# Kernel optimization log

Hardware: AMD Instinct MI355X
Metric: run time of the kernel (lower is better)

## Reference

```python
import jax, jax.numpy as jnp
import numpy as np

B, L, H, Q = 64, 512, 1024, 64
VA_H = 256


def setup_inputs() -> dict:
    key = jax.random.key(0)
    ks = jax.random.split(key, 10)
    hidden_states = jax.random.normal(ks[0], (B, L, H), dtype=jnp.float32)
    quad_spans = jax.random.randint(ks[1], (B, Q, 4), 0, L, dtype=jnp.int64)
    quad_mask = jnp.ones((B, Q), dtype=jnp.int32)
    s = 0.02
    W1 = jax.random.normal(ks[2], (3 * H, VA_H), dtype=jnp.float32) * s
    b1 = jnp.zeros((VA_H,), dtype=jnp.float32)
    W2 = jax.random.normal(ks[3], (VA_H, VA_H // 2), dtype=jnp.float32) * s
    b2 = jnp.zeros((VA_H // 2,), dtype=jnp.float32)
    W3 = jax.random.normal(ks[4], (VA_H // 2, 2), dtype=jnp.float32) * s
    b3 = jnp.zeros((2,), dtype=jnp.float32)
    return {"hidden_states": hidden_states, "quad_spans": quad_spans,
            "quad_mask": quad_mask, "W1": W1, "b1": b1, "W2": W2, "b2": b2,
            "W3": W3, "b3": b3}


def _pool_spans(hidden_states, quad_spans, quad_mask):
    # hidden_states [B,L,H]; quad_spans [B,Q,4]; quad_mask [B,Q]
    Bn, Ln, Hn = hidden_states.shape
    pos = jnp.arange(Ln)[None, None, :]                      # [1,1,L]
    asp_s = quad_spans[:, :, 0:1]
    asp_e = quad_spans[:, :, 1:2]
    opi_s = quad_spans[:, :, 2:3]
    opi_e = quad_spans[:, :, 3:4]
    asp_valid = asp_s >= 2
    opi_valid = opi_s >= 2
    sep = pos == 1                                           # [SEP] fallback
    asp_m = ((pos >= asp_s) & (pos <= asp_e) & asp_valid) | (~asp_valid & sep)
    opi_m = ((pos >= opi_s) & (pos <= opi_e) & opi_valid) | (~opi_valid & sep)
    qm = (quad_mask != 0)[:, :, None]
    asp_f = (asp_m & qm).astype(hidden_states.dtype)         # [B,Q,L]
    opi_f = (opi_m & qm).astype(hidden_states.dtype)
    h_asp = jnp.einsum('bql,blh->bqh', asp_f, hidden_states) / jnp.clip(
        asp_f.sum(-1, keepdims=True), 1.0, None)
    h_opi = jnp.einsum('bql,blh->bqh', opi_f, hidden_states) / jnp.clip(
        opi_f.sum(-1, keepdims=True), 1.0, None)
    return h_asp, h_opi


def reference(hidden_states, quad_spans, quad_mask, W1, b1, W2, b2, W3, b3):
    h_asp, h_opi = _pool_spans(hidden_states, quad_spans, quad_mask)
    h_pair = jnp.concatenate([h_asp, h_opi, h_asp * h_opi], axis=-1)  # [B,Q,3H]
    x = jax.nn.gelu(h_pair @ W1 + b1, approximate=False)   # torch GELU = exact
    x = jax.nn.gelu(x @ W2 + b2, approximate=False)        # dropout: eval mode
    x = x @ W3 + b3                                        # [B,Q,2]
    va = jax.nn.sigmoid(x) * 8.0 + 1.0
    return va * quad_mask[:, :, None].astype(va.dtype)
```

## Files before the change

kernel.cpp:

```cpp
#include <hip/hip_runtime.h>
#include <math.h>


typedef __attribute__((ext_vector_type(4))) float f32x4;
typedef __attribute__((ext_vector_type(8))) short bf16x8;

#define NPAIR 4096
#define LSEQ 512
#define HDIM 1024

__device__ __forceinline__ unsigned int pack2(float lo, float hi) {
  const unsigned int a = __float_as_uint(lo) + 0x8000u;
  const unsigned int b = __float_as_uint(hi) + 0x8000u;
  return __builtin_amdgcn_perm(b, a, 0x07060302u);
}
__device__ __forceinline__ unsigned short f2bf(float f) {
  return (unsigned short)((__float_as_uint(f) + 0x8000u) >> 16);
}
__device__ __forceinline__ float gelu(float x) {
  return 0.5f * x * (1.f + erff(x * 0.70710678118654752f));
}

__global__ __launch_bounds__(256, 4) void pool_mfma_kernel(
    const float* __restrict__ hs, const int* __restrict__ spans,
    const int* __restrict__ qmask, unsigned short* __restrict__ hpair) {
  __shared__ __align__(16) unsigned char smem[34816];
  __shared__ float scl[128];
  typedef unsigned short BlT[64][40];
  BlT* Bl = (BlT*)smem;
  float(*S)[68] = (float(*)[68])smem;

  const int b = blockIdx.x >> 4;
  const int n0 = (blockIdx.x & 15) * 64;
  const int tid = threadIdx.x;
  const int lane = tid & 63;
  const int lm = lane & 15, quad = lane >> 4;
  const int wm = (tid >> 6) * 32;

  const bool is64 =
      (spans[1] == 0) && (spans[3] == 0) && (spans[5] == 0) && (spans[7] == 0);

  auto span_of = [&](int r, int& s, int& e) {
    const int q = r & 63, t = r >> 6;
    const int idx = (b * 64 + q) * 4 + t * 2;
    s = is64 ? spans[idx * 2] : spans[idx];
    e = is64 ? spans[idx * 2 + 2] : spans[idx + 1];
    if (s < 2) { s = 1; e = 1; }
  };
  int s0, e0, s1, e1;
  span_of(wm + lm, s0, e0);
  span_of(wm + 16 + lm, s1, e1);

  if (tid < 128) {
    int s, e;
    span_of(tid, s, e);
    const int c = (e >= s) ? (e - s + 1) : 0;
    const float sc = 1.f / (float)(c < 1 ? 1 : c);
    scl[tid] = (qmask[b * 64 + (tid & 63)] != 0) ? sc : 0.f;
  }

  f32x4 acc[2][4];
#pragma unroll
  for (int f = 0; f < 2; ++f)
#pragma unroll
    for (int g = 0; g < 4; ++g) acc[f][g] = f32x4{0.f, 0.f, 0.f, 0.f};

  const float* hsb = hs + (size_t)b * (LSEQ * HDIM);
  const int nl = tid & 63;
  const int kw = (tid >> 6) * 8;

  auto load8 = [&](int kbase, unsigned int (&tmp)[4]) {
    const float* src = hsb + (size_t)(kbase + kw) * HDIM + n0 + nl;
#pragma unroll
    for (int i = 0; i < 4; ++i) {
      const float f0 = src[(size_t)(2 * i) * HDIM];
      const float f1 = src[(size_t)(2 * i + 1) * HDIM];
      tmp[i] = pack2(f0, f1);
    }
  };

  unsigned int tmp[4];
  load8(0, tmp);
  *(uint4*)&Bl[0][nl][kw] = make_uint4(tmp[0], tmp[1], tmp[2], tmp[3]);

  for (int it = 0; it < 16; ++it) {
    const int k0 = it * 32;
    __syncthreads();
    if (it < 15) load8(k0 + 32, tmp);

    bf16x8 a0, a1;
#pragma unroll
    for (int j = 0; j < 8; ++j) {
      const int k = k0 + quad * 8 + j;
      a0[j] = (short)((k >= s0 && k <= e0) ? 0x3F80 : 0);
      a1[j] = (short)((k >= s1 && k <= e1) ? 0x3F80 : 0);
    }
    const BlT& Bc = Bl[it & 1];
#pragma unroll
    for (int g = 0; g < 4; ++g) {
      bf16x8 bg = *(const bf16x8*)&Bc[g * 16 + lm][quad * 8];
      acc[0][g] = __builtin_amdgcn_mfma_f32_16x16x32_bf16(a0, bg, acc[0][g], 0, 0, 0);
      acc[1][g] = __builtin_amdgcn_mfma_f32_16x16x32_bf16(a1, bg, acc[1][g], 0, 0, 0);
    }
    if (it < 15) {
      *(uint4*)&Bl[(it + 1) & 1][nl][kw] = make_uint4(tmp[0], tmp[1], tmp[2], tmp[3]);
    }
  }

  __syncthreads();
#pragma unroll
  for (int f = 0; f < 2; ++f)
#pragma unroll
    for (int g = 0; g < 4; ++g)
#pragma unroll
      for (int r = 0; r < 4; ++r)
        S[wm + f * 16 + quad * 4 + r][g * 16 + lm] = acc[f][g][r];
  __syncthreads();

  const int q = tid >> 2;
  const int cg = (tid & 3) * 16;
  const float sA = scl[q], sO = scl[64 + q];
  unsigned short* dst = hpair + (size_t)(b * 64 + q) * 3072 + n0 + cg;
#pragma unroll
  for (int h = 0; h < 2; ++h) {
    float a[8], o[8];
#pragma unroll
    for (int i = 0; i < 8; ++i) {
      a[i] = S[q][cg + h * 8 + i] * sA;
      o[i] = S[64 + q][cg + h * 8 + i] * sO;
    }
    uint4 wa, wo, wp;
    wa.x = pack2(a[0], a[1]); wa.y = pack2(a[2], a[3]);
    wa.z = pack2(a[4], a[5]); wa.w = pack2(a[6], a[7]);
    wo.x = pack2(o[0], o[1]); wo.y = pack2(o[2], o[3]);
    wo.z = pack2(o[4], o[5]); wo.w = pack2(o[6], o[7]);
    wp.x = pack2(a[0] * o[0], a[1] * o[1]); wp.y = pack2(a[2] * o[2], a[3] * o[3]);
    wp.z = pack2(a[4] * o[4], a[5] * o[5]); wp.w = pack2(a[6] * o[6], a[7] * o[7]);
    *(uint4*)(dst + h * 8) = wa;
    *(uint4*)(dst + 1024 + h * 8) = wo;
    *(uint4*)(dst + 2048 + h * 8) = wp;
  }
}

__global__ void transpose_two(const float* __restrict__ W1,
                              unsigned short* __restrict__ W1T,
                              const float* __restrict__ W2,
                              unsigned short* __restrict__ W2T) {
  __shared__ float t[32][33];
  const float* in;
  unsigned short* out;
  int R, C, c0, r0;
  int blk = blockIdx.x;
  if (blk < 768) {
    in = W1; out = W1T; R = 3072; C = 256;
    c0 = (blk & 7) * 32; r0 = (blk >> 3) * 32;
  } else {
    blk -= 768;
    in = W2; out = W2T; R = 256; C = 128;
    c0 = (blk & 3) * 32; r0 = (blk >> 2) * 32;
  }
  const int x = threadIdx.x, y = threadIdx.y;
#pragma unroll
  for (int i = 0; i < 32; i += 8)
    t[y + i][x] = in[(size_t)(r0 + y + i) * C + c0 + x];
  __syncthreads();
#pragma unroll
  for (int i = 0; i < 32; i += 8)
    out[(size_t)(c0 + y + i) * R + r0 + x] = f2bf(t[x][y + i]);
}

__global__ __launch_bounds__(256) void gemm_bt_partial(
    const unsigned short* __restrict__ A, const unsigned short* __restrict__ Bt,
    float* __restrict__ P, int M, int N, int K, int KH) {
  __shared__ __align__(16) unsigned short Al[64][40];
  __shared__ __align__(16) unsigned short Bl[64][40];
  const int bm = blockIdx.x * 64, bn = blockIdx.y * 64;
  const int kz = blockIdx.z * KH;
  const int tid = threadIdx.x;
  const int wave = tid >> 6, lane = tid & 63;
  const int wm = (wave & 1) * 32, wn = (wave >> 1) * 32;
  const int ar = tid >> 2, ac = (tid & 3) * 8;
  const int lm = lane & 15, lk = (lane >> 4) * 8;

  f32x4 acc00 = {0.f, 0.f, 0.f, 0.f}, acc01 = {0.f, 0.f, 0.f, 0.f};
  f32x4 acc10 = {0.f, 0.f, 0.f, 0.f}, acc11 = {0.f, 0.f, 0.f, 0.f};

  const unsigned short* pa = A + (size_t)(bm + ar) * K + kz + ac;
  const unsigned short* pb = Bt + (size_t)(bn + ar) * K + kz + ac;

  for (int k0 = 0; k0 < KH; k0 += 32) {
    uint4 va = *(const uint4*)(pa + k0);
    uint4 vb = *(const uint4*)(pb + k0);
    *(uint4*)&Al[ar][ac] = va;
    *(uint4*)&Bl[ar][ac] = vb;
    __syncthreads();
    bf16x8 a0 = *(const bf16x8*)&Al[wm + lm][lk];
    bf16x8 a1 = *(const bf16x8*)&Al[wm + 16 + lm][lk];
    bf16x8 b0 = *(const bf16x8*)&Bl[wn + lm][lk];
    bf16x8 b1 = *(const bf16x8*)&Bl[wn + 16 + lm][lk];
    acc00 = __builtin_amdgcn_mfma_f32_16x16x32_bf16(a0, b0, acc00, 0, 0, 0);
    acc01 = __builtin_amdgcn_mfma_f32_16x16x32_bf16(a0, b1, acc01, 0, 0, 0);
    acc10 = __builtin_amdgcn_mfma_f32_16x16x32_bf16(a1, b0, acc10, 0, 0, 0);
    acc11 = __builtin_amdgcn_mfma_f32_16x16x32_bf16(a1, b1, acc11, 0, 0, 0);
    __syncthreads();
  }

  float* Pz = P + (size_t)blockIdx.z * M * N;
  const int r0 = bm + wm + ((lane >> 4) << 2);
  const int c0 = bn + wn + lm;
  auto emit = [&](f32x4 v, int row0, int col) {
#pragma unroll
    for (int r = 0; r < 4; ++r) Pz[(size_t)(row0 + r) * N + col] = v[r];
  };
  emit(acc00, r0, c0);
  emit(acc10, r0 + 16, c0);
  emit(acc01, r0, c0 + 16);
  emit(acc11, r0 + 16, c0 + 16);
}

__global__ __launch_bounds__(256) void gemm2_head_kernel(
    const float* __restrict__ P, const unsigned short* __restrict__ Bt,
    const float* __restrict__ b1, const float* __restrict__ b2,
    const float* __restrict__ W3, const float* __restrict__ b3,
    const int* __restrict__ qmask, float* __restrict__ out) {
  __shared__ __align__(16) unsigned short Al[64][40];
  __shared__ __align__(16) unsigned short Bl[128][40];
  __shared__ float S2[64][129];
  __shared__ float w3[256];

  const int bm = blockIdx.x * 64;
  const int tid = threadIdx.x;
  const int wave = tid >> 6, lane = tid & 63;
  const int wm = (wave & 1) * 32, wn = (wave >> 1) * 64;
  const int ar = tid >> 2, ac = (tid & 3) * 8;
  const int br = tid >> 1, bc = (tid & 1) * 16;
  const int lm = lane & 15, quad = lane >> 4;

  w3[tid] = W3[tid];

  f32x4 acc[2][4];
#pragma unroll
  for (int f = 0; f < 2; ++f)
#pragma unroll
    for (int g = 0; g < 4; ++g) acc[f][g] = f32x4{0.f, 0.f, 0.f, 0.f};

  const float* p0 = P + (size_t)(bm + ar) * 256 + ac;
  const float* p1 = p0 + (size_t)NPAIR * 256;
  const unsigned short* pb = Bt + (size_t)br * 256 + bc;

  for (int k0 = 0; k0 < 256; k0 += 32) {
    float4 u0 = *(const float4*)(p0 + k0);
    float4 u1 = *(const float4*)(p0 + k0 + 4);
    float4 v0 = *(const float4*)(p1 + k0);
    float4 v1 = *(const float4*)(p1 + k0 + 4);
    float4 bb0 = *(const float4*)(b1 + k0 + ac);
    float4 bb1 = *(const float4*)(b1 + k0 + ac + 4);
    const float g0 = gelu(u0.x + v0.x + bb0.x), g1 = gelu(u0.y + v0.y + bb0.y);
    const float g2 = gelu(u0.z + v0.z + bb0.z), g3 = gelu(u0.w + v0.w + bb0.w);
    const float g4 = gelu(u1.x + v1.x + bb1.x), g5 = gelu(u1.y + v1.y + bb1.y);
    const float g6 = gelu(u1.z + v1.z + bb1.z), g7 = gelu(u1.w + v1.w + bb1.w);
    uint4 va;
    va.x = pack2(g0, g1); va.y = pack2(g2, g3);
    va.z = pack2(g4, g5); va.w = pack2(g6, g7);
    uint4 vb0 = *(const uint4*)(pb + k0);
    uint4 vb1 = *(const uint4*)(pb + k0 + 8);
    *(uint4*)&Al[ar][ac] = va;
    *(uint4*)&Bl[br][bc] = vb0;
    *(uint4*)&Bl[br][bc + 8] = vb1;
    __syncthreads();
    bf16x8 a0 = *(const bf16x8*)&Al[wm + lm][quad * 8];
    bf16x8 a1 = *(const bf16x8*)&Al[wm + 16 + lm][quad * 8];
#pragma unroll
    for (int g = 0; g < 4; ++g) {
      bf16x8 bg = *(const bf16x8*)&Bl[wn + g * 16 + lm][quad * 8];
      acc[0][g] = __builtin_amdgcn_mfma_f32_16x16x32_bf16(a0, bg, acc[0][g], 0, 0, 0);
      acc[1][g] = __builtin_amdgcn_mfma_f32_16x16x32_bf16(a1, bg, acc[1][g], 0, 0, 0);
    }
    __syncthreads();
  }

#pragma unroll
  for (int f = 0; f < 2; ++f)
#pragma unroll
    for (int g = 0; g < 4; ++g) {
      const int col = wn + g * 16 + lm;
#pragma unroll
      for (int r = 0; r < 4; ++r) {
        const int row = wm + f * 16 + quad * 4 + r;
        S2[row][col] = gelu(acc[f][g][r] + b2[col]);
      }
    }
  __syncthreads();

  if (tid < 128) {
    const int row = tid >> 1, o = tid & 1;
    float a = b3[o];
#pragma unroll 8
    for (int c = 0; c < 128; ++c) a += S2[row][c] * w3[c * 2 + o];
    const int pair = bm + row;
    const float qmf = (float)qmask[pair];
    out[pair * 2 + o] = ((1.f / (1.f + expf(-a))) * 8.f + 1.f) * qmf;
  }
}

extern "C" void kernel_launch(void* const* d_in, const int* in_sizes, int n_in,
                              void* d_out, int out_size, void* d_ws,
                              size_t ws_size, hipStream_t stream) {
  const float* hs = (const float*)d_in[0];
  const int* spans = (const int*)d_in[1];
  const int* qmask = (const int*)d_in[2];
  const float* W1 = (const float*)d_in[3];
  const float* b1 = (const float*)d_in[4];
  const float* W2 = (const float*)d_in[5];
  const float* b2 = (const float*)d_in[6];
  const float* W3 = (const float*)d_in[7];
  const float* b3 = (const float*)d_in[8];
  float* out = (float*)d_out;

  const size_t HPAIR_B = 25165824;
  const size_t P_B = 8388608;
  const size_t W1T_B = 1572864;

  char* ws = (char*)d_ws;
  size_t off = 0;
  unsigned short* hpair = (unsigned short*)(ws + off); off += HPAIR_B;
  float* P = (float*)(ws + off);                       off += P_B;
  unsigned short* W1T = (unsigned short*)(ws + off);   off += W1T_B;
  unsigned short* W2T = (unsigned short*)(ws + off);

  transpose_two<<<800, dim3(32, 8), 0, stream>>>(W1, W1T, W2, W2T);
  pool_mfma_kernel<<<1024, 256, 0, stream>>>(hs, spans, qmask, hpair);
  gemm_bt_partial<<<dim3(64, 4, 2), 256, 0, stream>>>(hpair, W1T, P, NPAIR,
                                                      256, 3072, 1536);
  gemm2_head_kernel<<<64, 256, 0, stream>>>(P, W2T, b1, b2, W3, b3, qmask,
                                            out);
}
```

Measured before the change: 254.3 us.

## Use direct global-to-LDS loads in GEMM1 and split bias+GELU reduction kernel

The first GEMM now stages its A/B tiles with global_load_lds, which writes straight into unpadded LDS and skips the round trip through registers. A scalar fallback is kept for when the builtin is missing. The split-K reduction, bias add and GELU are pulled out of the second GEMM into a separate elementwise kernel that writes bf16 activations, so GEMM2's 64 blocks read compact bf16 instead of doing the GELU work themselves. This costs one extra launch and an extra round trip through a 2 MB buffer, and removing the LDS padding may cause bank conflicts on the MFMA fragment reads.

```diff
diff --git a/kernel.cpp b/kernel.cpp
--- a/kernel.cpp
+++ b/kernel.cpp
@@ -8,6 +8,15 @@
 #define NPAIR 4096
 #define LSEQ 512
 #define HDIM 1024
+
+#if defined(__has_builtin)
+#if __has_builtin(__builtin_amdgcn_global_load_lds)
+#define HAVE_GLDS 1
+#endif
+#endif
+#ifndef HAVE_GLDS
+#define HAVE_GLDS 0
+#endif
 
 __device__ __forceinline__ unsigned int pack2(float lo, float hi) {
   const unsigned int a = __float_as_uint(lo) + 0x8000u;
@@ -172,27 +181,33 @@
 __global__ __launch_bounds__(256) void gemm_bt_partial(
     const unsigned short* __restrict__ A, const unsigned short* __restrict__ Bt,
     float* __restrict__ P, int M, int N, int K, int KH) {
-  __shared__ __align__(16) unsigned short Al[64][40];
-  __shared__ __align__(16) unsigned short Bl[64][40];
+  __shared__ __align__(16) unsigned short Al[64][32];
+  __shared__ __align__(16) unsigned short Bl[64][32];
   const int bm = blockIdx.x * 64, bn = blockIdx.y * 64;
   const int kz = blockIdx.z * KH;
   const int tid = threadIdx.x;
   const int wave = tid >> 6, lane = tid & 63;
   const int wm = (wave & 1) * 32, wn = (wave >> 1) * 32;
-  const int ar = tid >> 2, ac = (tid & 3) * 8;
   const int lm = lane & 15, lk = (lane >> 4) * 8;
+
+  const int srow = wave * 16 + (lane >> 2);
+  const int scol = (lane & 3) * 8;
+  const unsigned short* ga = A + (size_t)(bm + srow) * K + kz + scol;
+  const unsigned short* gb = Bt + (size_t)(bn + srow) * K + kz + scol;
+  unsigned short* la = &Al[0][0] + wave * 512;
+  unsigned short* lb = &Bl[0][0] + wave * 512;
 
   f32x4 acc00 = {0.f, 0.f, 0.f, 0.f}, acc01 = {0.f, 0.f, 0.f, 0.f};
   f32x4 acc10 = {0.f, 0.f, 0.f, 0.f}, acc11 = {0.f, 0.f, 0.f, 0.f};
 
-  const unsigned short* pa = A + (size_t)(bm + ar) * K + kz + ac;
-  const unsigned short* pb = Bt + (size_t)(bn + ar) * K + kz + ac;
-
   for (int k0 = 0; k0 < KH; k0 += 32) {
-    uint4 va = *(const uint4*)(pa + k0);
-    uint4 vb = *(const uint4*)(pb + k0);
-    *(uint4*)&Al[ar][ac] = va;
-    *(uint4*)&Bl[ar][ac] = vb;
+#if HAVE_GLDS
+    __builtin_amdgcn_global_load_lds(ga + k0, la, 16, 0, 0);
+    __builtin_amdgcn_global_load_lds(gb + k0, lb, 16, 0, 0);
+#else
+    *(uint4*)(la + lane * 8) = *(const uint4*)(ga + k0);
+    *(uint4*)(lb + lane * 8) = *(const uint4*)(gb + k0);
+#endif
     __syncthreads();
     bf16x8 a0 = *(const bf16x8*)&Al[wm + lm][lk];
     bf16x8 a1 = *(const bf16x8*)&Al[wm + 16 + lm][lk];
@@ -218,11 +233,29 @@
   emit(acc11, r0 + 16, c0 + 16);
 }
 
+__global__ __launch_bounds__(256) void reduce_bias_gelu(
+    const float* __restrict__ P, const float* __restrict__ bias,
+    unsigned short* __restrict__ X) {
+  const int t = blockIdx.x * 256 + threadIdx.x;
+  const int e = t * 4;
+  float4 p0 = *(const float4*)(P + e);
+  float4 p1 = *(const float4*)(P + (size_t)NPAIR * 256 + e);
+  float4 bs = *(const float4*)(bias + (e & 255));
+  const float v0 = gelu(p0.x + p1.x + bs.x);
+  const float v1 = gelu(p0.y + p1.y + bs.y);
+  const float v2 = gelu(p0.z + p1.z + bs.z);
+  const float v3 = gelu(p0.w + p1.w + bs.w);
+  uint2 w;
+  w.x = pack2(v0, v1);
+  w.y = pack2(v2, v3);
+  *(uint2*)(X + e) = w;
+}
+
 __global__ __launch_bounds__(256) void gemm2_head_kernel(
-    const float* __restrict__ P, const unsigned short* __restrict__ Bt,
-    const float* __restrict__ b1, const float* __restrict__ b2,
-    const float* __restrict__ W3, const float* __restrict__ b3,
-    const int* __restrict__ qmask, float* __restrict__ out) {
+    const unsigned short* __restrict__ A, const unsigned short* __restrict__ Bt,
+    const float* __restrict__ b2, const float* __restrict__ W3,
+    const float* __restrict__ b3, const int* __restrict__ qmask,
+    float* __restrict__ out) {
   __shared__ __align__(16) unsigned short Al[64][40];
   __shared__ __align__(16) unsigned short Bl[128][40];
   __shared__ float S2[64][129];
@@ -244,24 +277,11 @@
 #pragma unroll
     for (int g = 0; g < 4; ++g) acc[f][g] = f32x4{0.f, 0.f, 0.f, 0.f};
 
-  const float* p0 = P + (size_t)(bm + ar) * 256 + ac;
-  const float* p1 = p0 + (size_t)NPAIR * 256;
+  const unsigned short* pa = A + (size_t)(bm + ar) * 256 + ac;
   const unsigned short* pb = Bt + (size_t)br * 256 + bc;
 
   for (int k0 = 0; k0 < 256; k0 += 32) {
-    float4 u0 = *(const float4*)(p0 + k0);
-    float4 u1 = *(const float4*)(p0 + k0 + 4);
-    float4 v0 = *(const float4*)(p1 + k0);
-    float4 v1 = *(const float4*)(p1 + k0 + 4);
-    float4 bb0 = *(const float4*)(b1 + k0 + ac);
-    float4 bb1 = *(const float4*)(b1 + k0 + ac + 4);
-    const float g0 = gelu(u0.x + v0.x + bb0.x), g1 = gelu(u0.y + v0.y + bb0.y);
-    const float g2 = gelu(u0.z + v0.z + bb0.z), g3 = gelu(u0.w + v0.w + bb0.w);
-    const float g4 = gelu(u1.x + v1.x + bb1.x), g5 = gelu(u1.y + v1.y + bb1.y);
-    const float g6 = gelu(u1.z + v1.z + bb1.z), g7 = gelu(u1.w + v1.w + bb1.w);
-    uint4 va;
-    va.x = pack2(g0, g1); va.y = pack2(g2, g3);
-    va.z = pack2(g4, g5); va.w = pack2(g6, g7);
+    uint4 va = *(const uint4*)(pa + k0);
     uint4 vb0 = *(const uint4*)(pb + k0);
     uint4 vb1 = *(const uint4*)(pb + k0 + 8);
     *(uint4*)&Al[ar][ac] = va;
@@ -318,12 +338,14 @@
   float* out = (float*)d_out;
 
   const size_t HPAIR_B = 25165824;
+  const size_t X1_B = 2097152;
   const size_t P_B = 8388608;
   const size_t W1T_B = 1572864;
 
   char* ws = (char*)d_ws;
   size_t off = 0;
   unsigned short* hpair = (unsigned short*)(ws + off); off += HPAIR_B;
+  unsigned short* x1 = (unsigned short*)(ws + off);    off += X1_B;
   float* P = (float*)(ws + off);                       off += P_B;
   unsigned short* W1T = (unsigned short*)(ws + off);   off += W1T_B;
   unsigned short* W2T = (unsigned short*)(ws + off);
@@ -332,6 +354,6 @@
   pool_mfma_kernel<<<1024, 256, 0, stream>>>(hs, spans, qmask, hpair);
   gemm_bt_partial<<<dim3(64, 4, 2), 256, 0, stream>>>(hpair, W1T, P, NPAIR,
                                                       256, 3072, 1536);
-  gemm2_head_kernel<<<64, 256, 0, stream>>>(P, W2T, b1, b2, W3, b3, qmask,
-                                            out);
-}
+  reduce_bias_gelu<<<1024, 256, 0, stream>>>(P, b1, x1);
+  gemm2_head_kernel<<<64, 256, 0, stream>>>(x1, W2T, b2, W3, b3, qmask, out);
+}
```

After: 248.3 us. 2.4% less time.
